# Kernel tuning notes

Measured on AMD Instinct MI355X. Metric: run time of the kernel, lower is better.

The kernel has to match this reference:

```python
import jax, jax.numpy as jnp
import numpy as np

HIDDEN = 2048
N_HEADS = 16
N_KV_HEADS = 4
HEAD_DIM = HIDDEN // N_HEADS  # 128
ROPE_THETA = 10000.0


def setup_inputs() -> dict:
    key = jax.random.key(0)
    ks = jax.random.split(key, 5)
    B, S = 2, 2048
    scale = 0.02
    return {
        "hidden_states": jax.random.normal(ks[0], (B, S, HIDDEN), jnp.float32),
        "Wq": jax.random.normal(ks[1], (HIDDEN, N_HEADS * HEAD_DIM), jnp.float32) * scale,
        "Wk": jax.random.normal(ks[2], (HIDDEN, N_KV_HEADS * HEAD_DIM), jnp.float32) * scale,
        "Wv": jax.random.normal(ks[3], (HIDDEN, N_KV_HEADS * HEAD_DIM), jnp.float32) * scale,
        "Wo": jax.random.normal(ks[4], (HIDDEN, HIDDEN), jnp.float32) * scale,
    }


def _rope_tables(seq_len, dim, dtype):
    inv_freq = 1.0 / (ROPE_THETA ** (jnp.arange(0, dim, 2, dtype=jnp.float32) / dim))
    t = jnp.arange(seq_len, dtype=jnp.float32)
    freqs = jnp.outer(t, inv_freq)            # [S, dim/2]
    emb = jnp.concatenate([freqs, freqs], -1)  # [S, dim]
    return jnp.cos(emb).astype(dtype), jnp.sin(emb).astype(dtype)


def _rotate_half(x):
    d = x.shape[-1] // 2
    return jnp.concatenate([-x[..., d:], x[..., :d]], axis=-1)


def _mqa_forward(hidden_states, Wq, Wk, Wv, Wo):
    B, S, _ = hidden_states.shape
    q = (hidden_states @ Wq).reshape(B, S, N_HEADS, HEAD_DIM).transpose(0, 2, 1, 3)      # [B,H,S,D]
    k = (hidden_states @ Wk).reshape(B, S, N_KV_HEADS, HEAD_DIM).transpose(0, 2, 1, 3)   # [B,Hkv,S,D]
    v = (hidden_states @ Wv).reshape(B, S, N_KV_HEADS, HEAD_DIM).transpose(0, 2, 1, 3)

    cos, sin = _rope_tables(S, HEAD_DIM, q.dtype)  # [S,D]
    q = q * cos + _rotate_half(q) * sin
    k = k * cos + _rotate_half(k) * sin

    # GQA: group query heads over shared KV heads instead of repeat_kv (same math)
    g = N_HEADS // N_KV_HEADS
    qg = q.reshape(B, N_KV_HEADS, g, S, HEAD_DIM)
    scale = 1.0 / np.sqrt(HEAD_DIM)
    scores = jnp.einsum("bhgqd,bhkd->bhgqk", qg, k) * scale  # [B,Hkv,g,S,S]
    causal = jnp.tril(jnp.ones((S, S), bool))
    scores = jnp.where(causal, scores, -jnp.inf)
    probs = jax.nn.softmax(scores.astype(jnp.float32), axis=-1).astype(q.dtype)
    out = jnp.einsum("bhgqk,bhkd->bhgqd", probs, v)  # [B,Hkv,g,S,D]
    out = out.reshape(B, N_HEADS, S, HEAD_DIM).transpose(0, 2, 1, 3).reshape(B, S, HIDDEN)
    return out @ Wo


def reference(hidden_states, Wq, Wk, Wv, Wo):
    return _mqa_forward(hidden_states, Wq, Wk, Wv, Wo)
```

## Files before the change

### kernel.cpp

```cpp
#include <hip/hip_runtime.h>
#include <hip/hip_bf16.h>
#include <cstdint>
#include <cstddef>

#define HIDDEN   2048
#define NH       16
#define NKV      4
#define HD       128
#define SEQ      2048
#define BATCH    2
#define NTOK     (BATCH*SEQ)
#define QKV_LD   3072
#define KOFF     2048
#define VOFF     2560
#define SM_SCALE 0.08838834764831845f
#define LOG2E    1.4426950408889634f

typedef __attribute__((ext_vector_type(8)))  short bf16x8;
typedef __attribute__((ext_vector_type(4)))  float f32x4v;
typedef __attribute__((ext_vector_type(16))) float f32x16;
typedef unsigned short ushort_t;

__device__ __forceinline__ unsigned short f2bf(float f) {
  return __builtin_bit_cast(unsigned short, __float2bfloat16(f));
}
__device__ __forceinline__ float bf2f(ushort_t u) {
  return __builtin_bit_cast(float, (unsigned)u << 16);
}
__device__ __forceinline__ unsigned pack2(float a, float b) {
  return (unsigned)f2bf(a) | ((unsigned)f2bf(b) << 16);
}

__device__ __forceinline__ void gload16(const void* g, void* l) {
  __builtin_amdgcn_global_load_lds(
      (const __attribute__((address_space(1))) unsigned int*)g,
      (__attribute__((address_space(3))) unsigned int*)l, 16, 0, 0);
}

__global__ __launch_bounds__(256) void conv_f2b(
    const float* __restrict__ in, ushort_t* __restrict__ out, int n8)
{
  const int i = blockIdx.x*256 + threadIdx.x;
  if (i >= n8) return;
  const float4 a = ((const float4*)in)[2*i];
  const float4 b = ((const float4*)in)[2*i + 1];
  uint4 r;
  r.x = pack2(a.x, a.y); r.y = pack2(a.z, a.w);
  r.z = pack2(b.x, b.y); r.w = pack2(b.z, b.w);
  ((uint4*)out)[i] = r;
}

__global__ __launch_bounds__(256) void transpose_f2b(
    const float* __restrict__ W, ushort_t* __restrict__ Wt, int K, int N)
{
  __shared__ float tile[32][33];
  const int n0 = blockIdx.x*32, k0 = blockIdx.y*32;
  const int tx = threadIdx.x & 31, ty = threadIdx.x >> 5;
  #pragma unroll
  for (int i = 0; i < 4; ++i)
    tile[ty*4 + i][tx] = W[(size_t)(k0 + ty*4 + i)*N + n0 + tx];
  __syncthreads();
  #pragma unroll
  for (int i = 0; i < 4; ++i) {
    const int nl = ty*4 + i;
    Wt[(size_t)(n0 + nl)*K + k0 + tx] = f2bf(tile[tx][nl]);
  }
}

template<bool B16OUT>
__global__ __launch_bounds__(256) void bt_gemm(
    const ushort_t* __restrict__ A, const ushort_t* __restrict__ Bt,
    void* __restrict__ Cv, int ldc)
{
  __shared__ ushort_t As[128*64];
  __shared__ ushort_t Bs[128*64];
  const int t = threadIdx.x, lane = t & 63, w = t >> 6;
  const int bm = blockIdx.y*128, bn = blockIdx.x*128;
  const int wr = w >> 1, wc = w & 1;
  const int lr = lane & 15, lg = lane >> 4;

  f32x4v acc[4][4];
  #pragma unroll
  for (int fm = 0; fm < 4; ++fm)
    #pragma unroll
    for (int fn = 0; fn < 4; ++fn)
      #pragma unroll
      for (int r = 0; r < 4; ++r) acc[fm][fn][r] = 0.f;

  const char* Ab = (const char*)A;
  const char* Bb = (const char*)Bt;
  char* asb = (char*)As;
  char* bsb = (char*)Bs;

  for (int kt = 0; kt < HIDDEN*2; kt += 128) {
    __syncthreads();
    #pragma unroll
    for (int u = 0; u < 4; ++u) {
      const int idx = u*256 + t;
      const int row = idx >> 3;
      const int kb  = (idx & 7) * 16;
      const int skb = kb ^ ((row & 7) << 4);
      gload16(Ab + (size_t)(bm + row)*4096 + kt + skb, asb + idx*16);
      gload16(Bb + (size_t)(bn + row)*4096 + kt + skb, bsb + idx*16);
    }
    __syncthreads();
    #pragma unroll
    for (int kc = 0; kc < 2; ++kc) {
      bf16x8 af[4], bfr[4];
      #pragma unroll
      for (int f = 0; f < 4; ++f) {
        const int rm = wr*64 + f*16 + lr;
        af[f]  = *(const bf16x8*)(asb + rm*128 + ((kc*64 + lg*16) ^ ((rm & 7) << 4)));
        const int rn = wc*64 + f*16 + lr;
        bfr[f] = *(const bf16x8*)(bsb + rn*128 + ((kc*64 + lg*16) ^ ((rn & 7) << 4)));
      }
      #pragma unroll
      for (int fm = 0; fm < 4; ++fm)
        #pragma unroll
        for (int fn = 0; fn < 4; ++fn)
          acc[fm][fn] = __builtin_amdgcn_mfma_f32_16x16x32_bf16(af[fm], bfr[fn], acc[fm][fn], 0, 0, 0);
    }
  }

  #pragma unroll
  for (int fm = 0; fm < 4; ++fm) {
    const int m = bm + wr*64 + fm*16 + lg*4;
    #pragma unroll
    for (int fn = 0; fn < 4; ++fn) {
      const int n = bn + wc*64 + fn*16 + lr;
      #pragma unroll
      for (int r = 0; r < 4; ++r) {
        if constexpr (B16OUT)
          ((ushort_t*)Cv)[(size_t)(m + r)*ldc + n] = f2bf(acc[fm][fn][r]);
        else
          ((float*)Cv)[(size_t)(m + r)*ldc + n] = acc[fm][fn][r];
      }
    }
  }
}

__global__ __launch_bounds__(256) void rope_conv(
    const ushort_t* __restrict__ QKVb, ushort_t* __restrict__ Qo,
    ushort_t* __restrict__ Ko)
{
  const int total = NTOK * (NH + NKV) * (HD/2);
  int idx = blockIdx.x * 256 + threadIdx.x;
  if (idx >= total) return;
  const int i   = idx & 63;
  int tmp = idx >> 6;
  const int hs  = tmp % (NH + NKV);
  const int tkn = tmp / (NH + NKV);
  const int s   = tkn & (SEQ - 1);
  const int b   = tkn >> 11;
  const float invf = expf(-(float)i * 0.14391156831212787f);
  float sn, cs;
  sincosf((float)s * invf, &sn, &cs);
  const size_t base = (size_t)tkn * QKV_LD + (hs < NH ? hs * HD : KOFF + (hs - NH) * HD);
  const float x0 = bf2f(QKVb[base + i]);
  const float x1 = bf2f(QKVb[base + i + 64]);
  const float y0 = x0 * cs - x1 * sn;
  const float y1 = x1 * cs + x0 * sn;
  if (hs < NH) {
    ushort_t* q = Qo + (size_t)tkn * HIDDEN + hs * HD;
    q[i]      = f2bf(y0 * (SM_SCALE * LOG2E));
    q[i + 64] = f2bf(y1 * (SM_SCALE * LOG2E));
  } else {
    ushort_t* k = Ko + ((size_t)(b*NKV + (hs - NH))*SEQ + s) * HD;
    k[i]      = f2bf(y0);
    k[i + 64] = f2bf(y1);
  }
}

__global__ __launch_bounds__(256) void vt_conv(
    const ushort_t* __restrict__ QKVb, ushort_t* __restrict__ Vtb)
{
  __shared__ ushort_t tile[32][33];
  const int s0 = blockIdx.x*32;
  const int d0 = (blockIdx.y & 3)*32;
  const int bk = blockIdx.y >> 2;
  const int b = bk >> 2, hk = bk & 3;
  const int tx = threadIdx.x & 31, ty = threadIdx.x >> 5;
  #pragma unroll
  for (int i = 0; i < 4; ++i) {
    const int sl = ty*4 + i;
    tile[sl][tx] = QKVb[(size_t)(b*SEQ + s0 + sl)*QKV_LD + VOFF + hk*HD + d0 + tx];
  }
  __syncthreads();
  #pragma unroll
  for (int i = 0; i < 4; ++i) {
    const int dl = ty*4 + i;
    Vtb[((size_t)bk*HD + d0 + dl)*SEQ + s0 + tx] = tile[tx][dl];
  }
}

__global__ __launch_bounds__(256) void attn_mfma11(
    const ushort_t* __restrict__ Qb, const ushort_t* __restrict__ Kb,
    const ushort_t* __restrict__ Vtb, ushort_t* __restrict__ O)
{
  __shared__ char smem[65536];

  const int bx = blockIdx.x;
  const int qt = 63 - (int)blockIdx.y;
  const int b = bx >> 2, hk = bx & 3;
  const int t = threadIdx.x, w = t >> 6, lane = t & 63;
  const int c = lane & 31, hi = lane >> 5;
  const int h = hk*4 + w;
  const int qw0 = qt*32;
  const int qg  = qw0 + c;
  const int nsteps = (qt + 2) >> 1;

  const char* Kbb = (const char*)(Kb + (size_t)(b*NKV + hk)*SEQ*HD);
  const char* Vbb = (const char*)(Vtb + (size_t)(b*NKV + hk)*HD*SEQ);

  int ksrc[4], vsrc[4], ldst[4];
  #pragma unroll
  for (int u = 0; u < 4; ++u) {
    const int idx = u*256 + t;
    const int krow = idx >> 4, kof = (idx & 15) << 4;
    ksrc[u] = krow*256 + (kof ^ ((krow & 15) << 4));
    const int vd = idx >> 3,  vof = (idx & 7) << 4;
    vsrc[u] = vd*(SEQ*2) + (vof ^ ((vd & 7) << 4));
    ldst[u] = idx*16;
  }

  bf16x8 qf[8];
  {
    const ushort_t* qrow = Qb + (size_t)(b*SEQ + qg)*HIDDEN + h*HD;
    #pragma unroll
    for (int kc = 0; kc < 8; ++kc)
      qf[kc] = *(const bf16x8*)(qrow + kc*16 + hi*8);
  }

  f32x16 ot[4];
  #pragma unroll
  for (int nc = 0; nc < 4; ++nc)
    #pragma unroll
    for (int r = 0; r < 16; ++r) ot[nc][r] = 0.f;
  float m = -1e30f, l = 0.f;

  #pragma unroll
  for (int u = 0; u < 4; ++u) {
    gload16(Kbb + ksrc[u], smem + ldst[u]);
    gload16(Vbb + vsrc[u], smem + 32768 + ldst[u]);
  }
  __syncthreads();

  int cur = 0;
  for (int kt = 0; kt < nsteps; ++kt) {
    if (kt + 1 < nsteps) {
      const int nb = cur ^ 1;
      const size_t kto = (size_t)(kt + 1) * 16384;
      const int    vto = (kt + 1) * 128;
      #pragma unroll
      for (int u = 0; u < 4; ++u) {
        gload16(Kbb + kto + ksrc[u], smem + nb*16384 + ldst[u]);
        gload16(Vbb + vto + vsrc[u], smem + 32768 + nb*16384 + ldst[u]);
      }
    }
    const char* klds = smem + cur*16384;
    const char* vlds = smem + 32768 + cur*16384;
    f32x16 s[2];
    #pragma unroll
    for (int kn = 0; kn < 2; ++kn)
      #pragma unroll
      for (int r = 0; r < 16; ++r) s[kn][r] = 0.f;
    #pragma unroll
    for (int kn = 0; kn < 2; ++kn) {
      const int row = kn*32 + c;
      const int sw = (row & 15) << 4;
      #pragma unroll
      for (int kc = 0; kc < 8; ++kc) {
        const bf16x8 ka = *(const bf16x8*)(klds + row*256 + ((kc*32 + hi*16) ^ sw));
        s[kn] = __builtin_amdgcn_mfma_f32_32x32x16_bf16(ka, qf[kc], s[kn], 0, 0, 0);
      }
    }
    if (kt == nsteps - 1) {
      #pragma unroll
      for (int kn = 0; kn < 2; ++kn)
        #pragma unroll
        for (int r = 0; r < 16; ++r) {
          const int kg_ = kt*64 + kn*32 + (r & 3) + 8*(r >> 2) + 4*hi;
          if (kg_ > qg) s[kn][r] = -1e30f;
        }
    }
    float mx[16];
    #pragma unroll
    for (int r = 0; r < 16; ++r) mx[r] = fmaxf(s[0][r], s[1][r]);
    #pragma unroll
    for (int st = 8; st > 0; st >>= 1)
      #pragma unroll
      for (int r = 0; r < 8; ++r)
        if (r < st) mx[r] = fmaxf(mx[r], mx[r + st]);
    const float pm = fmaxf(mx[0], __shfl_xor(mx[0], 32));
    if (!__all(pm - m <= 8.f)) {
      const float mnew = fmaxf(m, pm);
      const float corr = exp2f(m - mnew);
      m = mnew;
      l *= corr;
      #pragma unroll
      for (int nc = 0; nc < 4; ++nc) ot[nc] *= corr;
    }
    float ls = 0.f;
    #pragma unroll
    for (int kn = 0; kn < 2; ++kn)
      #pragma unroll
      for (int r = 0; r < 16; ++r) {
        const float p = exp2f(s[kn][r] - m);
        ls += p;
        s[kn][r] = p;
      }
    l += ls;
    #pragma unroll
    for (int kn = 0; kn < 2; ++kn) {
      #pragma unroll
      for (int rem = 0; rem < 2; ++rem) {
        const int base = 8*rem;
        const unsigned A0 = pack2(s[kn][base+0], s[kn][base+1]);
        const unsigned A1 = pack2(s[kn][base+2], s[kn][base+3]);
        const unsigned B0 = pack2(s[kn][base+4], s[kn][base+5]);
        const unsigned B1 = pack2(s[kn][base+6], s[kn][base+7]);
        const unsigned u  = hi ? A0 : B0;
        const unsigned v  = hi ? A1 : B1;
        const unsigned su = (unsigned)__shfl_xor((int)u, 32);
        const unsigned sv = (unsigned)__shfl_xor((int)v, 32);
        uint4 wv;
        wv.x = hi ? su : A0;
        wv.y = hi ? sv : A1;
        wv.z = hi ? B0 : su;
        wv.w = hi ? B1 : sv;
        const bf16x8 pb = __builtin_bit_cast(bf16x8, wv);
        const int kc = kn*2 + rem;
        #pragma unroll
        for (int nc = 0; nc < 4; ++nc) {
          const int dim = nc*32 + c;
          const bf16x8 va = *(const bf16x8*)(vlds + dim*128 + ((kc*32 + hi*16) ^ ((dim & 7) << 4)));
          ot[nc] = __builtin_amdgcn_mfma_f32_32x32x16_bf16(va, pb, ot[nc], 0, 0, 0);
        }
      }
    }
    __syncthreads();
    cur ^= 1;
  }

  const float lt = l + __shfl_xor(l, 32);
  const float inv = 1.f / lt;
  ushort_t* orow = O + (size_t)(b*SEQ + qg) * HIDDEN + h*HD;
  #pragma unroll
  for (int nc = 0; nc < 4; ++nc)
    #pragma unroll
    for (int r = 0; r < 16; r += 2) {
      const int dim = nc*32 + (r & 3) + 8*(r >> 2) + 4*hi;
      *(unsigned*)(orow + dim) = pack2(ot[nc][r]*inv, ot[nc][r+1]*inv);
    }
}

extern "C" void kernel_launch(void* const* d_in, const int* in_sizes, int n_in,
                              void* d_out, int out_size, void* d_ws, size_t ws_size,
                              hipStream_t stream)
{
  (void)in_sizes; (void)n_in; (void)out_size; (void)ws_size;
  const float* H  = (const float*)d_in[0];
  const float* Wq = (const float*)d_in[1];
  const float* Wk = (const float*)d_in[2];
  const float* Wv = (const float*)d_in[3];
  const float* Wo = (const float*)d_in[4];
  float* out = (float*)d_out;

  char* ws = (char*)d_ws;
  ushort_t* QKVb = (ushort_t*)ws;
  ushort_t* Hb   = (ushort_t*)(ws + 25165824);
  ushort_t* Qb   = Hb;
  ushort_t* Wt   = (ushort_t*)(ws + 41943040);
  ushort_t* Kb   = (ushort_t*)(ws + 54525952);
  ushort_t* Vtb  = (ushort_t*)(ws + 58720256);
  ushort_t* Oat  = (ushort_t*)(ws + 62914560);

  conv_f2b<<<4096, 256, 0, stream>>>(H, Hb, NTOK*HIDDEN/8);
  transpose_f2b<<<dim3(64, 64), 256, 0, stream>>>(Wq, Wt,                     2048, 2048);
  transpose_f2b<<<dim3(16, 64), 256, 0, stream>>>(Wk, Wt + (size_t)2048*2048, 2048, 512);
  transpose_f2b<<<dim3(16, 64), 256, 0, stream>>>(Wv, Wt + (size_t)2560*2048, 2048, 512);

  bt_gemm<true><<<dim3(QKV_LD/128, NTOK/128), 256, 0, stream>>>(Hb, Wt, QKVb, QKV_LD);

  const int rope_total = NTOK * (NH + NKV) * (HD/2);
  rope_conv<<<(rope_total + 255)/256, 256, 0, stream>>>(QKVb, Qb, Kb);
  vt_conv<<<dim3(SEQ/32, 32), 256, 0, stream>>>(QKVb, Vtb);

  attn_mfma11<<<dim3(8, 64), 256, 0, stream>>>(Qb, Kb, Vtb, Oat);

  transpose_f2b<<<dim3(64, 64), 256, 0, stream>>>(Wo, Wt, 2048, 2048);
  bt_gemm<false><<<dim3(HIDDEN/128, NTOK/128), 256, 0, stream>>>(Oat, Wt, out, HIDDEN);
}
```

Before: 238.2 us.

## Replace GEMM with larger-tile double-buffered 512-thread kernel

```diff
diff --git a/kernel.cpp b/kernel.cpp
--- a/kernel.cpp
+++ b/kernel.cpp
@@ -67,73 +67,116 @@
   }
 }
 
-template<bool B16OUT>
-__global__ __launch_bounds__(256) void bt_gemm(
+template<int BN, bool B16OUT>
+__global__ __launch_bounds__(512, 1) void bt_gemm2(
     const ushort_t* __restrict__ A, const ushort_t* __restrict__ Bt,
     void* __restrict__ Cv, int ldc)
 {
-  __shared__ ushort_t As[128*64];
-  __shared__ ushort_t Bs[128*64];
+  constexpr int WN = BN/64;
+  constexpr int WM = 8/WN;
+  constexpr int MF = 16/WM;
+  constexpr int BROUNDS = BN/64;
+  constexpr int BUFB = 32768 + BN*128;
+  __shared__ char smem[2*BUFB];
+
   const int t = threadIdx.x, lane = t & 63, w = t >> 6;
-  const int bm = blockIdx.y*128, bn = blockIdx.x*128;
-  const int wr = w >> 1, wc = w & 1;
+  const int wm = w / WN, wn = w % WN;
+  const int bm = blockIdx.y*256, bn = blockIdx.x*BN;
   const int lr = lane & 15, lg = lane >> 4;
 
-  f32x4v acc[4][4];
-  #pragma unroll
-  for (int fm = 0; fm < 4; ++fm)
-    #pragma unroll
-    for (int fn = 0; fn < 4; ++fn)
-      #pragma unroll
-      for (int r = 0; r < 4; ++r) acc[fm][fn][r] = 0.f;
+  f32x4v acc[MF][4];
+  #pragma unroll
+  for (int mf = 0; mf < MF; ++mf)
+    #pragma unroll
+    for (int nf = 0; nf < 4; ++nf)
+      #pragma unroll
+      for (int r = 0; r < 4; ++r) acc[mf][nf][r] = 0.f;
 
   const char* Ab = (const char*)A;
   const char* Bb = (const char*)Bt;
-  char* asb = (char*)As;
-  char* bsb = (char*)Bs;
-
-  for (int kt = 0; kt < HIDDEN*2; kt += 128) {
+
+  auto stage = [&](int kt2, int d) {
+    char* ab = smem + d*BUFB;
+    char* bb = ab + 32768;
+    const int ktb = kt2*128;
+    #pragma unroll
+    for (int u = 0; u < 4; ++u) {
+      const int idx = u*512 + t;
+      const int row = idx >> 3;
+      const int kb  = ((idx & 7)*16) ^ ((row & 7) << 4);
+      gload16(Ab + (size_t)(bm + row)*4096 + ktb + kb, ab + idx*16);
+    }
+    #pragma unroll
+    for (int u = 0; u < BROUNDS; ++u) {
+      const int idx = u*512 + t;
+      const int row = idx >> 3;
+      const int kb  = ((idx & 7)*16) ^ ((row & 7) << 4);
+      gload16(Bb + (size_t)(bn + row)*4096 + ktb + kb, bb + idx*16);
+    }
+  };
+
+  stage(0, 0);
+  __syncthreads();
+
+#define PHASE(q) { \
+    bf16x8 af0k0, af0k1, af1k0, af1k1; \
+    { const int rm = wm*(MF*16) + (2*(q))*16 + lr; \
+      const char* ap = asp + rm*128; \
+      const int sw = (rm & 7) << 4; \
+      af0k0 = *(const bf16x8*)(ap + ((lg*16) ^ sw)); \
+      af0k1 = *(const bf16x8*)(ap + ((64 + lg*16) ^ sw)); } \
+    { const int rm = wm*(MF*16) + (2*(q)+1)*16 + lr; \
+      const char* ap = asp + rm*128; \
+      const int sw = (rm & 7) << 4; \
+      af1k0 = *(const bf16x8*)(ap + ((lg*16) ^ sw)); \
+      af1k1 = *(const bf16x8*)(ap + ((64 + lg*16) ^ sw)); } \
+    __builtin_amdgcn_s_setprio(1); \
+    _Pragma("unroll") \
+    for (int nf = 0; nf < 4; ++nf) { \
+      acc[2*(q)][nf]   = __builtin_amdgcn_mfma_f32_16x16x32_bf16(af0k0, bfr[nf][0], acc[2*(q)][nf],   0,0,0); \
+      acc[2*(q)][nf]   = __builtin_amdgcn_mfma_f32_16x16x32_bf16(af0k1, bfr[nf][1], acc[2*(q)][nf],   0,0,0); \
+      acc[2*(q)+1][nf] = __builtin_amdgcn_mfma_f32_16x16x32_bf16(af1k0, bfr[nf][0], acc[2*(q)+1][nf], 0,0,0); \
+      acc[2*(q)+1][nf] = __builtin_amdgcn_mfma_f32_16x16x32_bf16(af1k1, bfr[nf][1], acc[2*(q)+1][nf], 0,0,0); \
+    } \
+    __builtin_amdgcn_s_setprio(0); }
+
+  int cur = 0;
+  for (int kt = 0; kt < 32; ++kt) {
+    if (kt < 31) stage(kt + 1, cur ^ 1);
+    const char* asp = smem + cur*BUFB;
+    const char* bsp = asp + 32768;
+    bf16x8 bfr[4][2];
+    #pragma unroll
+    for (int nf = 0; nf < 4; ++nf) {
+      const int rn = wn*64 + nf*16 + lr;
+      const char* bp = bsp + rn*128;
+      const int sw = (rn & 7) << 4;
+      bfr[nf][0] = *(const bf16x8*)(bp + ((lg*16) ^ sw));
+      bfr[nf][1] = *(const bf16x8*)(bp + ((64 + lg*16) ^ sw));
+    }
+    PHASE(0)
+    PHASE(1)
+    if constexpr (MF == 8) {
+      PHASE(2)
+      PHASE(3)
+    }
     __syncthreads();
-    #pragma unroll
-    for (int u = 0; u < 4; ++u) {
-      const int idx = u*256 + t;
-      const int row = idx >> 3;
-      const int kb  = (idx & 7) * 16;
-      const int skb = kb ^ ((row & 7) << 4);
-      gload16(Ab + (size_t)(bm + row)*4096 + kt + skb, asb + idx*16);
-      gload16(Bb + (size_t)(bn + row)*4096 + kt + skb, bsb + idx*16);
-    }
-    __syncthreads();
-    #pragma unroll
-    for (int kc = 0; kc < 2; ++kc) {
-      bf16x8 af[4], bfr[4];
-      #pragma unroll
-      for (int f = 0; f < 4; ++f) {
-        const int rm = wr*64 + f*16 + lr;
-        af[f]  = *(const bf16x8*)(asb + rm*128 + ((kc*64 + lg*16) ^ ((rm & 7) << 4)));
-        const int rn = wc*64 + f*16 + lr;
-        bfr[f] = *(const bf16x8*)(bsb + rn*128 + ((kc*64 + lg*16) ^ ((rn & 7) << 4)));
-      }
-      #pragma unroll
-      for (int fm = 0; fm < 4; ++fm)
-        #pragma unroll
-        for (int fn = 0; fn < 4; ++fn)
-          acc[fm][fn] = __builtin_amdgcn_mfma_f32_16x16x32_bf16(af[fm], bfr[fn], acc[fm][fn], 0, 0, 0);
-    }
-  }
-
-  #pragma unroll
-  for (int fm = 0; fm < 4; ++fm) {
-    const int m = bm + wr*64 + fm*16 + lg*4;
-    #pragma unroll
-    for (int fn = 0; fn < 4; ++fn) {
-      const int n = bn + wc*64 + fn*16 + lr;
+    cur ^= 1;
+  }
+#undef PHASE
+
+  #pragma unroll
+  for (int mf = 0; mf < MF; ++mf) {
+    const int m = bm + wm*(MF*16) + mf*16 + lg*4;
+    #pragma unroll
+    for (int nf = 0; nf < 4; ++nf) {
+      const int n = bn + wn*64 + nf*16 + lr;
       #pragma unroll
       for (int r = 0; r < 4; ++r) {
         if constexpr (B16OUT)
-          ((ushort_t*)Cv)[(size_t)(m + r)*ldc + n] = f2bf(acc[fm][fn][r]);
+          ((ushort_t*)Cv)[(size_t)(m + r)*ldc + n] = f2bf(acc[mf][nf][r]);
         else
-          ((float*)Cv)[(size_t)(m + r)*ldc + n] = acc[fm][fn][r];
+          ((float*)Cv)[(size_t)(m + r)*ldc + n] = acc[mf][nf][r];
       }
     }
   }
@@ -380,7 +423,7 @@
   transpose_f2b<<<dim3(16, 64), 256, 0, stream>>>(Wk, Wt + (size_t)2048*2048, 2048, 512);
   transpose_f2b<<<dim3(16, 64), 256, 0, stream>>>(Wv, Wt + (size_t)2560*2048, 2048, 512);
 
-  bt_gemm<true><<<dim3(QKV_LD/128, NTOK/128), 256, 0, stream>>>(Hb, Wt, QKVb, QKV_LD);
+  bt_gemm2<256, true><<<dim3(QKV_LD/256, NTOK/256), 512, 0, stream>>>(Hb, Wt, QKVb, QKV_LD);
 
   const int rope_total = NTOK * (NH + NKV) * (HD/2);
   rope_conv<<<(rope_total + 255)/256, 256, 0, stream>>>(QKVb, Qb, Kb);
@@ -389,5 +432,5 @@
   attn_mfma11<<<dim3(8, 64), 256, 0, stream>>>(Qb, Kb, Vtb, Oat);
 
   transpose_f2b<<<dim3(64, 64), 256, 0, stream>>>(Wo, Wt, 2048, 2048);
-  bt_gemm<false><<<dim3(HIDDEN/128, NTOK/128), 256, 0, stream>>>(Oat, Wt, out, HIDDEN);
-}
+  bt_gemm2<128, false><<<dim3(HIDDEN/128, NTOK/256), 512, 0, stream>>>(Oat, Wt, out, HIDDEN);
+}
```

After: 211.2 us. 11.3% less time.
